# Kernel tuning notes

Hardware: AMD Instinct MI355X
Metric: run time of the kernel (lower is better)

The kernel has to match this reference:

```python
import jax, jax.numpy as jnp
import numpy as np

N_HEAD, D_MODEL, D_HEAD = 16, 1024, 64
LN_EPS = 1e-5
SCALE = 1.0 / (D_HEAD ** 0.5)


def _rel_shift(x):
    # x: [qlen, klen, bsz, n_head]
    q, k, b, n = x.shape
    zero_pad = jnp.zeros((q, 1, b, n), x.dtype)
    x_padded = jnp.concatenate([zero_pad, x], axis=1)        # [q, k+1, b, n]
    x_padded = x_padded.reshape(k + 1, q, b, n)
    return x_padded[1:].reshape(q, k, b, n)


def setup_inputs() -> dict:
    key = jax.random.key(0)
    ks = jax.random.split(key, 8)
    qlen, bsz = 2048, 4
    H = N_HEAD * D_HEAD
    s = 0.02
    return {
        "w": jax.random.normal(ks[0], (qlen, bsz, D_MODEL), jnp.float32),
        "r": jax.random.normal(ks[1], (qlen, D_MODEL), jnp.float32),
        "qkv_w": jax.random.normal(ks[2], (3 * H, D_MODEL), jnp.float32) * s,
        "r_net_w": jax.random.normal(ks[3], (H, D_MODEL), jnp.float32) * s,
        "o_w": jax.random.normal(ks[4], (D_MODEL, H), jnp.float32) * s,
        "r_w_bias": jax.random.normal(ks[5], (N_HEAD, D_HEAD), jnp.float32) * s,
        "r_r_bias": jax.random.normal(ks[6], (N_HEAD, D_HEAD), jnp.float32) * s,
        "ln_g": jnp.ones((D_MODEL,), jnp.float32),
        "ln_b": jnp.zeros((D_MODEL,), jnp.float32),
    }


def _layer_norm(x, g, b):
    mu = jnp.mean(x, axis=-1, keepdims=True)
    var = jnp.var(x, axis=-1, keepdims=True)
    return (x - mu) * jax.lax.rsqrt(var + LN_EPS) * g + b


def reference(w, r, qkv_w, r_net_w, o_w, r_w_bias, r_r_bias, ln_g, ln_b):
    qlen, bsz, _ = w.shape
    rlen = r.shape[0]
    H = N_HEAD * D_HEAD

    w_heads = jnp.einsum('ibm,hm->ibh', w, qkv_w)            # [q,b,3H]
    r_head_k = jnp.einsum('jm,hm->jh', r, r_net_w)           # [r,H]

    w_head_q = w_heads[..., :H].reshape(qlen, bsz, N_HEAD, D_HEAD)
    w_head_k = w_heads[..., H:2 * H].reshape(qlen, bsz, N_HEAD, D_HEAD)
    w_head_v = w_heads[..., 2 * H:].reshape(qlen, bsz, N_HEAD, D_HEAD)
    r_head_k = r_head_k.reshape(rlen, N_HEAD, D_HEAD)

    AC = jnp.einsum('ibnd,jbnd->ijbn', w_head_q + r_w_bias, w_head_k)
    BD = jnp.einsum('ibnd,jnd->ijbn', w_head_q + r_r_bias, r_head_k)
    BD = _rel_shift(BD)

    attn_score = (AC + BD) * SCALE                           # [q,k,b,n]
    attn_prob = jax.nn.softmax(attn_score, axis=1)

    attn_vec = jnp.einsum('ijbn,jbnd->ibnd', attn_prob, w_head_v)
    attn_vec = attn_vec.reshape(qlen, bsz, H)
    attn_out = jnp.einsum('ibh,mh->ibm', attn_vec, o_w)

    return _layer_norm(w + attn_out, ln_g, ln_b)
```

## Files before the change

kernel.cpp:

```cpp
#include <hip/hip_runtime.h>
#include <hip/hip_bf16.h>
#include <stdint.h>

using bf16 = __hip_bfloat16;
typedef __attribute__((ext_vector_type(8))) short bf16x8;
typedef __attribute__((ext_vector_type(4))) float f32x4;
typedef __attribute__((ext_vector_type(2))) int i32x2;

#define SCALE 0.125f

__device__ __forceinline__ float b2f(bf16 x) { return __bfloat162float(x); }
__device__ __forceinline__ bf16 f2b(float x) { return __float2bfloat16(x); }

__device__ __forceinline__ void gll16(const void* g, void* l) {
  __builtin_amdgcn_global_load_lds((const __attribute__((address_space(1))) void*)g,
                                   (__attribute__((address_space(3))) void*)l, 16, 0, 0);
}

__device__ __forceinline__ bf16x8 cat64(i32x2 a, i32x2 b) {
  int4 v; v.x = a.x; v.y = a.y; v.z = b.x; v.w = b.y;
  return *(bf16x8*)&v;
}

__global__ __launch_bounds__(256) void cvt_kernel(const float* __restrict__ in, bf16* __restrict__ out, int n4) {
  int i = blockIdx.x * 256 + threadIdx.x;
  if (i >= n4) return;
  float4 v = ((const float4*)in)[i];
  alignas(8) bf16 o[4];
  o[0] = f2b(v.x); o[1] = f2b(v.y); o[2] = f2b(v.z); o[3] = f2b(v.w);
  ((uint2*)out)[i] = *(const uint2*)o;
}

template<int STORE_BF16>
__global__ __launch_bounds__(256) void gemm_bt(const bf16* __restrict__ A, const bf16* __restrict__ B,
                                               void* __restrict__ C, int M, int N, int K) {
  __shared__ bf16 As[128][72];
  __shared__ bf16 Bs[128][72];
  const int tid = threadIdx.x;
  const int lane = tid & 63;
  const int w = tid >> 6, wr = w >> 1, wc = w & 1;
  const int m0 = blockIdx.y * 128, n0 = blockIdx.x * 128;
  const int lr = lane & 15, lg = lane >> 4;
  f32x4 acc[4][4] = {};
  for (int k0 = 0; k0 < K; k0 += 64) {
    __syncthreads();
#pragma unroll
    for (int i = 0; i < 4; ++i) {
      int c = tid + i * 256;
      int row = c >> 3, seg = c & 7;
      *(int4*)&As[row][seg * 8] = *(const int4*)&A[(size_t)(m0 + row) * K + k0 + seg * 8];
      *(int4*)&Bs[row][seg * 8] = *(const int4*)&B[(size_t)(n0 + row) * K + k0 + seg * 8];
    }
    __syncthreads();
#pragma unroll
    for (int kk = 0; kk < 2; ++kk) {
      bf16x8 af[4], bfv[4];
#pragma unroll
      for (int m = 0; m < 4; ++m) af[m] = *(const bf16x8*)&As[wr * 64 + m * 16 + lr][kk * 32 + lg * 8];
#pragma unroll
      for (int n = 0; n < 4; ++n) bfv[n] = *(const bf16x8*)&Bs[wc * 64 + n * 16 + lr][kk * 32 + lg * 8];
#pragma unroll
      for (int m = 0; m < 4; ++m)
#pragma unroll
        for (int n = 0; n < 4; ++n)
          acc[m][n] = __builtin_amdgcn_mfma_f32_16x16x32_bf16(af[m], bfv[n], acc[m][n], 0, 0, 0);
    }
  }
#pragma unroll
  for (int m = 0; m < 4; ++m)
#pragma unroll
    for (int n = 0; n < 4; ++n)
#pragma unroll
      for (int r = 0; r < 4; ++r) {
        int row = m0 + wr * 64 + m * 16 + lg * 4 + r;
        int col = n0 + wc * 64 + n * 16 + lr;
        if (STORE_BF16) ((bf16*)C)[(size_t)row * N + col] = f2b(acc[m][n][r]);
        else            ((float*)C)[(size_t)row * N + col] = acc[m][n][r];
      }
}

__global__ __launch_bounds__(256) void flash_kernel(const bf16* __restrict__ wh, const bf16* __restrict__ rk,
                                                    const float* __restrict__ rwb, const float* __restrict__ rrb,
                                                    bf16* __restrict__ av) {
  const int hid = blockIdx.x;
  const int xcd = hid & 7;
  const int idx = hid >> 3;
  const int bn = xcd + 8 * (idx >> 5);
  const int q0 = (idx & 31) * 64;
  const int b = bn >> 4, n = bn & 15;
  const int tid = threadIdx.x, lane = tid & 63, w = tid >> 6;
  const int lr = lane & 15, lg = lane >> 4;
  __shared__ bf16 VtA[2 * 4096];
  __shared__ bf16 Ps[64][32];
  __shared__ bf16 Tp[64][128];

  bf16x8 qf[2], qrf[2][2];
#pragma unroll
  for (int kk = 0; kk < 2; ++kk) {
    {
      int row = q0 + w * 16 + lr;
      int4 raw = *(const int4*)&wh[((size_t)row * 4 + b) * 3072 + n * 64 + kk * 32 + lg * 8];
      const bf16* rp = (const bf16*)&raw;
      alignas(16) bf16 ov[8];
#pragma unroll
      for (int e = 0; e < 8; ++e) ov[e] = f2b((b2f(rp[e]) + rwb[n * 64 + kk * 32 + lg * 8 + e]) * SCALE);
      qf[kk] = *(const bf16x8*)ov;
    }
#pragma unroll
    for (int ao = 0; ao < 2; ++ao) {
      int row = q0 + ao + w * 16 + lr; if (row > 2047) row = 2047;
      int4 raw = *(const int4*)&wh[((size_t)row * 4 + b) * 3072 + n * 64 + kk * 32 + lg * 8];
      const bf16* rp = (const bf16*)&raw;
      alignas(16) bf16 ov[8];
#pragma unroll
      for (int e = 0; e < 8; ++e) ov[e] = f2b((b2f(rp[e]) + rrb[n * 64 + kk * 32 + lg * 8 + e]) * SCALE);
      qrf[ao][kk] = *(const bf16x8*)ov;
    }
  }

  auto coords = [&](int u, int& pbase, int& sub) {
    int tt = 64 * u - q0;
    if (tt <= -64) { pbase = tt + 2048; sub = 0; } else { pbase = tt; sub = 2; }
  };

  auto panel_direct = [&](int pbase, int sub) {
    const int aidx = sub ? 1 : 0;
#pragma unroll
    for (int nt = 0; nt < 4; ++nt) {
      int c = pbase + nt * 16 + lr - sub;
      c = c < 0 ? 0 : (c > 2047 ? 2047 : c);
      f32x4 pacc = {};
      bf16x8 b0 = *(const bf16x8*)&rk[(size_t)c * 1024 + n * 64 + lg * 8];
      bf16x8 b1 = *(const bf16x8*)&rk[(size_t)c * 1024 + n * 64 + 32 + lg * 8];
      __builtin_amdgcn_s_setprio(1);
      pacc = __builtin_amdgcn_mfma_f32_16x16x32_bf16(qrf[aidx][0], b0, pacc, 0, 0, 0);
      pacc = __builtin_amdgcn_mfma_f32_16x16x32_bf16(qrf[aidx][1], b1, pacc, 0, 0, 0);
      __builtin_amdgcn_s_setprio(0);
      int cm = (pbase + nt * 16 + lr) & 127;
#pragma unroll
      for (int r = 0; r < 4; ++r) Tp[w * 16 + lg * 4 + r][cm] = f2b(pacc[r]);
    }
  };

  auto stage_v = [&](int j0, int bufi) {
#pragma unroll
    for (int i = 0; i < 2; ++i) {
      int c = tid + i * 256;
      int jj = ((c >> 3) & 15) * 4 + ((c >> 1) & 3);
      int d0 = (c >> 7) * 16 + (c & 1) * 8;
      gll16(&wh[((size_t)(j0 + jj) * 4 + b) * 3072 + 2048 + n * 64 + d0],
            &VtA[bufi * 4096 + (w * 64 + i * 256) * 8]);
    }
  };

  panel_direct(1984 - q0, 0);
  { int pb, sb; coords(0, pb, sb); panel_direct(pb, sb); }
  stage_v(0, 0);

  const unsigned vtb = (unsigned)(uintptr_t)(__attribute__((address_space(3))) bf16*)VtA
                       + (unsigned)(lg * 256 + lr * 2);
  const bf16* kbase = wh + (size_t)b * 3072 + 1024 + n * 64;

  float lrow[4] = {0.f, 0.f, 0.f, 0.f};
  f32x4 oacc[4] = {};

  __syncthreads();

  int buf = 0;
  for (int u = 0; u < 32; ++u) {
    const int j0 = u * 64;
    if (u < 31) stage_v(j0 + 64, buf ^ 1);

    float bd[4][4];
#pragma unroll
    for (int f = 0; f < 4; ++f) {
      int jj = j0 + f * 16 + lr;
#pragma unroll
      for (int r = 0; r < 4; ++r) {
        int i = q0 + w * 16 + lg * 4 + r;
        int uu = jj - i;
        if (uu != 1) {
          int cm = (uu >= 2 ? uu : uu - 1) & 127;
          bd[f][r] = b2f(Tp[w * 16 + lg * 4 + r][cm]);
        } else bd[f][r] = 0.f;
      }
    }
    f32x4 s[4] = {};
#pragma unroll
    for (int kk = 0; kk < 2; ++kk)
#pragma unroll
      for (int f = 0; f < 4; ++f) {
        bf16x8 kf = *(const bf16x8*)&kbase[(size_t)(j0 + f * 16 + lr) * 12288 + kk * 32 + lg * 8];
        __builtin_amdgcn_s_setprio(1);
        s[f] = __builtin_amdgcn_mfma_f32_16x16x32_bf16(qf[kk], kf, s[f], 0, 0, 0);
        __builtin_amdgcn_s_setprio(0);
      }
#pragma unroll
    for (int f = 0; f < 4; ++f)
#pragma unroll
      for (int r = 0; r < 4; ++r) {
        float p = __expf(s[f][r] + bd[f][r]);
        s[f][r] = p;
        lrow[r] += p;
      }
    {
      unsigned va = vtb + (unsigned)(buf << 13);
      i32x2 t0, t1, t2, t3, t4, t5, t6, t7;
      bf16x8 pf;
#define TRRD(d_, o_) asm volatile("ds_read_b64_tr_b16 %0, %1 offset:" o_ : "=v"(d_) : "v"(va))
#pragma unroll
      for (int f = 0; f < 2; ++f)
#pragma unroll
        for (int r = 0; r < 4; ++r) {
          int row = w * 16 + lg * 4 + r;
          Ps[row][(f * 16 + lr) ^ (lg << 3)] = f2b(s[f][r]);
        }
      pf = *(const bf16x8*)&Ps[w * 16 + lr][(lg ^ ((lr >> 2) & 3)) * 8];
      TRRD(t0, "0");    TRRD(t1, "128");
      TRRD(t2, "2048"); TRRD(t3, "2176");
      TRRD(t4, "4096"); TRRD(t5, "4224");
      TRRD(t6, "6144"); TRRD(t7, "6272");
      asm volatile("s_waitcnt lgkmcnt(0)" ::: "memory");
      __builtin_amdgcn_sched_barrier(0);
      __builtin_amdgcn_s_setprio(1);
      oacc[0] = __builtin_amdgcn_mfma_f32_16x16x32_bf16(pf, cat64(t0, t1), oacc[0], 0, 0, 0);
      oacc[1] = __builtin_amdgcn_mfma_f32_16x16x32_bf16(pf, cat64(t2, t3), oacc[1], 0, 0, 0);
      oacc[2] = __builtin_amdgcn_mfma_f32_16x16x32_bf16(pf, cat64(t4, t5), oacc[2], 0, 0, 0);
      oacc[3] = __builtin_amdgcn_mfma_f32_16x16x32_bf16(pf, cat64(t6, t7), oacc[3], 0, 0, 0);
      __builtin_amdgcn_s_setprio(0);
#pragma unroll
      for (int f = 2; f < 4; ++f)
#pragma unroll
        for (int r = 0; r < 4; ++r) {
          int row = w * 16 + lg * 4 + r;
          Ps[row][((f - 2) * 16 + lr) ^ (lg << 3)] = f2b(s[f][r]);
        }
      pf = *(const bf16x8*)&Ps[w * 16 + lr][(lg ^ ((lr >> 2) & 3)) * 8];
      TRRD(t0, "1024"); TRRD(t1, "1152");
      TRRD(t2, "3072"); TRRD(t3, "3200");
      TRRD(t4, "5120"); TRRD(t5, "5248");
      TRRD(t6, "7168"); TRRD(t7, "7296");
      asm volatile("s_waitcnt lgkmcnt(0)" ::: "memory");
      __builtin_amdgcn_sched_barrier(0);
      __builtin_amdgcn_s_setprio(1);
      oacc[0] = __builtin_amdgcn_mfma_f32_16x16x32_bf16(pf, cat64(t0, t1), oacc[0], 0, 0, 0);
      oacc[1] = __builtin_amdgcn_mfma_f32_16x16x32_bf16(pf, cat64(t2, t3), oacc[1], 0, 0, 0);
      oacc[2] = __builtin_amdgcn_mfma_f32_16x16x32_bf16(pf, cat64(t4, t5), oacc[2], 0, 0, 0);
      oacc[3] = __builtin_amdgcn_mfma_f32_16x16x32_bf16(pf, cat64(t6, t7), oacc[3], 0, 0, 0);
      __builtin_amdgcn_s_setprio(0);
#undef TRRD
    }
    if (u < 31) {
      int pb, sb; coords(u + 1, pb, sb);
      panel_direct(pb, sb);
    }
    __syncthreads();
    buf ^= 1;
  }
#pragma unroll
  for (int r = 0; r < 4; ++r)
#pragma unroll
    for (int msk = 1; msk <= 8; msk <<= 1) lrow[r] += __shfl_xor(lrow[r], msk);
#pragma unroll
  for (int df = 0; df < 4; ++df)
#pragma unroll
    for (int r = 0; r < 4; ++r) {
      int i = q0 + w * 16 + lg * 4 + r;
      av[((size_t)i * 4 + b) * 1024 + n * 64 + df * 16 + lr] = f2b(oacc[df][r] / lrow[r]);
    }
}

__global__ __launch_bounds__(256) void ln_kernel(const float* __restrict__ w, const float* __restrict__ ao,
                                                 const float* __restrict__ g, const float* __restrict__ bb,
                                                 float* __restrict__ out) {
  const int row = blockIdx.x;
  const int t = threadIdx.x;
  const float4 wv = ((const float4*)(w + (size_t)row * 1024))[t];
  const float4 av = ((const float4*)(ao + (size_t)row * 1024))[t];
  float x0 = wv.x + av.x, x1 = wv.y + av.y, x2 = wv.z + av.z, x3 = wv.w + av.w;
  float s1 = x0 + x1 + x2 + x3;
  float s2 = x0 * x0 + x1 * x1 + x2 * x2 + x3 * x3;
#pragma unroll
  for (int m = 1; m <= 32; m <<= 1) { s1 += __shfl_xor(s1, m); s2 += __shfl_xor(s2, m); }
  __shared__ float red[8];
  const int lane = t & 63, wv2 = t >> 6;
  if (lane == 0) { red[wv2] = s1; red[4 + wv2] = s2; }
  __syncthreads();
  s1 = red[0] + red[1] + red[2] + red[3];
  s2 = red[4] + red[5] + red[6] + red[7];
  const float mu = s1 * (1.f / 1024.f);
  const float var = s2 * (1.f / 1024.f) - mu * mu;
  const float rr = rsqrtf(var + 1e-5f);
  const float4 gv = ((const float4*)g)[t];
  const float4 bv = ((const float4*)bb)[t];
  float4 o;
  o.x = (x0 - mu) * rr * gv.x + bv.x;
  o.y = (x1 - mu) * rr * gv.y + bv.y;
  o.z = (x2 - mu) * rr * gv.z + bv.z;
  o.w = (x3 - mu) * rr * gv.w + bv.w;
  ((float4*)(out + (size_t)row * 1024))[t] = o;
}

extern "C" void kernel_launch(void* const* d_in, const int* in_sizes, int n_in,
                              void* d_out, int out_size, void* d_ws, size_t ws_size,
                              hipStream_t stream) {
  const float* w    = (const float*)d_in[0];
  const float* r    = (const float*)d_in[1];
  const float* qkvw = (const float*)d_in[2];
  const float* rnw  = (const float*)d_in[3];
  const float* ow   = (const float*)d_in[4];
  const float* rwb  = (const float*)d_in[5];
  const float* rrb  = (const float*)d_in[6];
  const float* lng  = (const float*)d_in[7];
  const float* lnb  = (const float*)d_in[8];
  float* out = (float*)d_out;

  char* ws = (char*)d_ws;
  size_t off = 0;
  auto alloc = [&](size_t bytes) -> char* {
    char* p = ws + off; off += (bytes + 255) & ~((size_t)255); return p;
  };
  bf16*  wb  = (bf16*)alloc((size_t)8192 * 1024 * 2);
  bf16*  qb  = (bf16*)alloc((size_t)3072 * 1024 * 2);
  bf16*  rb  = (bf16*)alloc((size_t)2048 * 1024 * 2);
  bf16*  rnb = (bf16*)alloc((size_t)1024 * 1024 * 2);
  bf16*  owb = (bf16*)alloc((size_t)1024 * 1024 * 2);
  bf16*  wh  = (bf16*)alloc((size_t)8192 * 3072 * 2);
  bf16*  rkb = (bf16*)alloc((size_t)2048 * 1024 * 2);
  bf16*  avb = (bf16*)alloc((size_t)8192 * 1024 * 2);
  float* ao  = (float*)alloc((size_t)8192 * 1024 * 4);

  auto cvt = [&](const float* in, bf16* o, size_t nelem) {
    int n4 = (int)(nelem / 4);
    cvt_kernel<<<dim3((n4 + 255) / 256), dim3(256), 0, stream>>>(in, o, n4);
  };
  cvt(w, wb, (size_t)8192 * 1024);
  cvt(qkvw, qb, (size_t)3072 * 1024);
  cvt(r, rb, (size_t)2048 * 1024);
  cvt(rnw, rnb, (size_t)1024 * 1024);
  cvt(ow, owb, (size_t)1024 * 1024);

  gemm_bt<1><<<dim3(3072 / 128, 8192 / 128), dim3(256), 0, stream>>>(wb, qb, wh, 8192, 3072, 1024);
  gemm_bt<1><<<dim3(1024 / 128, 2048 / 128), dim3(256), 0, stream>>>(rb, rnb, rkb, 2048, 1024, 1024);

  flash_kernel<<<dim3(2048), dim3(256), 0, stream>>>(wh, rkb, rwb, rrb, avb);

  gemm_bt<0><<<dim3(1024 / 128, 8192 / 128), dim3(256), 0, stream>>>(avb, owb, ao, 8192, 1024, 1024);
  ln_kernel<<<dim3(8192), dim3(256), 0, stream>>>(w, ao, lng, lnb, out);
}
```

Before: 719.5 us.

## Give each wave private V/P/T buffers and drop block barriers in flash loop

Restructures the attention loop so each wave stages its own V tile and keeps private P and positional-score panels in LDS. That removes the per-iteration __syncthreads, which becomes a vmcnt wait. The key step shrinks from 64 to 32 columns, and the rel-shift panel is filled in 32-column chunks. Each wave now loads the full V tile itself, roughly quadrupling V global traffic, and the shorter loop body halves the MFMA work per iteration.

```diff
diff --git a/kernel.cpp b/kernel.cpp
--- a/kernel.cpp
+++ b/kernel.cpp
@@ -90,9 +90,9 @@
   const int b = bn >> 4, n = bn & 15;
   const int tid = threadIdx.x, lane = tid & 63, w = tid >> 6;
   const int lr = lane & 15, lg = lane >> 4;
-  __shared__ bf16 VtA[2 * 4096];
-  __shared__ bf16 Ps[64][32];
-  __shared__ bf16 Tp[64][128];
+  __shared__ bf16 VtW[4][2][2048];
+  __shared__ bf16 Ps[4][16][32];
+  __shared__ bf16 Tp[4][16][128];
 
   bf16x8 qf[2], qrf[2][2];
 #pragma unroll
@@ -118,15 +118,12 @@
     }
   }
 
-  auto coords = [&](int u, int& pbase, int& sub) {
-    int tt = 64 * u - q0;
-    if (tt <= -64) { pbase = tt + 2048; sub = 0; } else { pbase = tt; sub = 2; }
-  };
-
-  auto panel_direct = [&](int pbase, int sub) {
+  auto fill32 = [&](int tt) {
+    int pbase, sub;
+    if (tt <= -32) { pbase = tt + 2048; sub = 0; } else { pbase = tt; sub = 2; }
     const int aidx = sub ? 1 : 0;
 #pragma unroll
-    for (int nt = 0; nt < 4; ++nt) {
+    for (int nt = 0; nt < 2; ++nt) {
       int c = pbase + nt * 16 + lr - sub;
       c = c < 0 ? 0 : (c > 2047 ? 2047 : c);
       f32x4 pacc = {};
@@ -138,88 +135,80 @@
       __builtin_amdgcn_s_setprio(0);
       int cm = (pbase + nt * 16 + lr) & 127;
 #pragma unroll
-      for (int r = 0; r < 4; ++r) Tp[w * 16 + lg * 4 + r][cm] = f2b(pacc[r]);
+      for (int r = 0; r < 4; ++r) Tp[w][lg * 4 + r][cm] = f2b(pacc[r]);
     }
   };
 
   auto stage_v = [&](int j0, int bufi) {
 #pragma unroll
-    for (int i = 0; i < 2; ++i) {
-      int c = tid + i * 256;
-      int jj = ((c >> 3) & 15) * 4 + ((c >> 1) & 3);
-      int d0 = (c >> 7) * 16 + (c & 1) * 8;
+    for (int call = 0; call < 4; ++call) {
+      int c = call * 64 + lane;
+      int jj = ((c >> 3) & 7) * 4 + ((c & 7) >> 1);
+      int d0 = call * 16 + (c & 1) * 8;
       gll16(&wh[((size_t)(j0 + jj) * 4 + b) * 3072 + 2048 + n * 64 + d0],
-            &VtA[bufi * 4096 + (w * 64 + i * 256) * 8]);
+            &VtW[w][bufi][call * 512]);
     }
   };
 
-  panel_direct(1984 - q0, 0);
-  { int pb, sb; coords(0, pb, sb); panel_direct(pb, sb); }
+  fill32(-64 - q0);
+  fill32(-32 - q0);
+  fill32(0 - q0);
   stage_v(0, 0);
 
-  const unsigned vtb = (unsigned)(uintptr_t)(__attribute__((address_space(3))) bf16*)VtA
+  const unsigned vtb = (unsigned)(uintptr_t)(__attribute__((address_space(3))) bf16*)&VtW[w][0][0]
                        + (unsigned)(lg * 256 + lr * 2);
   const bf16* kbase = wh + (size_t)b * 3072 + 1024 + n * 64;
 
   float lrow[4] = {0.f, 0.f, 0.f, 0.f};
   f32x4 oacc[4] = {};
 
-  __syncthreads();
-
   int buf = 0;
-  for (int u = 0; u < 32; ++u) {
-    const int j0 = u * 64;
-    if (u < 31) stage_v(j0 + 64, buf ^ 1);
-
-    float bd[4][4];
-#pragma unroll
-    for (int f = 0; f < 4; ++f) {
-      int jj = j0 + f * 16 + lr;
-#pragma unroll
-      for (int r = 0; r < 4; ++r) {
-        int i = q0 + w * 16 + lg * 4 + r;
-        int uu = jj - i;
-        if (uu != 1) {
-          int cm = (uu >= 2 ? uu : uu - 1) & 127;
-          bd[f][r] = b2f(Tp[w * 16 + lg * 4 + r][cm]);
-        } else bd[f][r] = 0.f;
-      }
-    }
-    f32x4 s[4] = {};
+  for (int u2 = 0; u2 < 64; ++u2) {
+    const int j0 = u2 * 32;
+
+    f32x4 s[2] = {};
 #pragma unroll
     for (int kk = 0; kk < 2; ++kk)
 #pragma unroll
-      for (int f = 0; f < 4; ++f) {
+      for (int f = 0; f < 2; ++f) {
         bf16x8 kf = *(const bf16x8*)&kbase[(size_t)(j0 + f * 16 + lr) * 12288 + kk * 32 + lg * 8];
         __builtin_amdgcn_s_setprio(1);
         s[f] = __builtin_amdgcn_mfma_f32_16x16x32_bf16(qf[kk], kf, s[f], 0, 0, 0);
         __builtin_amdgcn_s_setprio(0);
       }
 #pragma unroll
-    for (int f = 0; f < 4; ++f)
+    for (int f = 0; f < 2; ++f) {
+      int jj = j0 + f * 16 + lr;
 #pragma unroll
       for (int r = 0; r < 4; ++r) {
-        float p = __expf(s[f][r] + bd[f][r]);
+        int i = q0 + w * 16 + lg * 4 + r;
+        int uu = jj - i;
+        float bd = 0.f;
+        if (uu != 1) {
+          int cm = (uu >= 2 ? uu : uu - 1) & 127;
+          bd = b2f(Tp[w][lg * 4 + r][cm]);
+        }
+        float p = __expf(s[f][r] + bd);
         s[f][r] = p;
         lrow[r] += p;
       }
+    }
+#pragma unroll
+    for (int f = 0; f < 2; ++f)
+#pragma unroll
+      for (int r = 0; r < 4; ++r)
+        Ps[w][lg * 4 + r][(f * 16 + lr) ^ (lg << 3)] = f2b(s[f][r]);
+    bf16x8 pf = *(const bf16x8*)&Ps[w][lr][(lg ^ ((lr >> 2) & 3)) * 8];
     {
-      unsigned va = vtb + (unsigned)(buf << 13);
+      unsigned va = vtb + (unsigned)(buf << 12);
       i32x2 t0, t1, t2, t3, t4, t5, t6, t7;
-      bf16x8 pf;
+      asm volatile("s_waitcnt vmcnt(0)" ::: "memory");
 #define TRRD(d_, o_) asm volatile("ds_read_b64_tr_b16 %0, %1 offset:" o_ : "=v"(d_) : "v"(va))
-#pragma unroll
-      for (int f = 0; f < 2; ++f)
-#pragma unroll
-        for (int r = 0; r < 4; ++r) {
-          int row = w * 16 + lg * 4 + r;
-          Ps[row][(f * 16 + lr) ^ (lg << 3)] = f2b(s[f][r]);
-        }
-      pf = *(const bf16x8*)&Ps[w * 16 + lr][(lg ^ ((lr >> 2) & 3)) * 8];
       TRRD(t0, "0");    TRRD(t1, "128");
-      TRRD(t2, "2048"); TRRD(t3, "2176");
-      TRRD(t4, "4096"); TRRD(t5, "4224");
-      TRRD(t6, "6144"); TRRD(t7, "6272");
+      TRRD(t2, "1024"); TRRD(t3, "1152");
+      TRRD(t4, "2048"); TRRD(t5, "2176");
+      TRRD(t6, "3072"); TRRD(t7, "3200");
+#undef TRRD
       asm volatile("s_waitcnt lgkmcnt(0)" ::: "memory");
       __builtin_amdgcn_sched_barrier(0);
       __builtin_amdgcn_s_setprio(1);
@@ -228,33 +217,11 @@
       oacc[2] = __builtin_amdgcn_mfma_f32_16x16x32_bf16(pf, cat64(t4, t5), oacc[2], 0, 0, 0);
       oacc[3] = __builtin_amdgcn_mfma_f32_16x16x32_bf16(pf, cat64(t6, t7), oacc[3], 0, 0, 0);
       __builtin_amdgcn_s_setprio(0);
-#pragma unroll
-      for (int f = 2; f < 4; ++f)
-#pragma unroll
-        for (int r = 0; r < 4; ++r) {
-          int row = w * 16 + lg * 4 + r;
-          Ps[row][((f - 2) * 16 + lr) ^ (lg << 3)] = f2b(s[f][r]);
-        }
-      pf = *(const bf16x8*)&Ps[w * 16 + lr][(lg ^ ((lr >> 2) & 3)) * 8];
-      TRRD(t0, "1024"); TRRD(t1, "1152");
-      TRRD(t2, "3072"); TRRD(t3, "3200");
-      TRRD(t4, "5120"); TRRD(t5, "5248");
-      TRRD(t6, "7168"); TRRD(t7, "7296");
-      asm volatile("s_waitcnt lgkmcnt(0)" ::: "memory");
-      __builtin_amdgcn_sched_barrier(0);
-      __builtin_amdgcn_s_setprio(1);
-      oacc[0] = __builtin_amdgcn_mfma_f32_16x16x32_bf16(pf, cat64(t0, t1), oacc[0], 0, 0, 0);
-      oacc[1] = __builtin_amdgcn_mfma_f32_16x16x32_bf16(pf, cat64(t2, t3), oacc[1], 0, 0, 0);
-      oacc[2] = __builtin_amdgcn_mfma_f32_16x16x32_bf16(pf, cat64(t4, t5), oacc[2], 0, 0, 0);
-      oacc[3] = __builtin_amdgcn_mfma_f32_16x16x32_bf16(pf, cat64(t6, t7), oacc[3], 0, 0, 0);
-      __builtin_amdgcn_s_setprio(0);
-#undef TRRD
-    }
-    if (u < 31) {
-      int pb, sb; coords(u + 1, pb, sb);
-      panel_direct(pb, sb);
-    }
-    __syncthreads();
+    }
+    if (u2 < 63) {
+      fill32(32 * (u2 + 1) - q0);
+      stage_v(j0 + 32, buf ^ 1);
+    }
     buf ^= 1;
   }
 #pragma unroll
```

Result: slower. 762.7 us (+6.0%).
